# Kernel optimization log

Measured on AMD Instinct MI355X. Metric: run time of the kernel, lower is better.

Reference implementation:

```python
import jax, jax.numpy as jnp
import numpy as np

EPS = 1e-6  # torch GaussianNLLLoss default eps


def _linear_params(key, in_size, out_size):
    # torch nn.Linear default init: U(-1/sqrt(in), 1/sqrt(in)) for W and b
    kw, kb = jax.random.split(key)
    bound = 1.0 / np.sqrt(in_size)
    W = jax.random.uniform(kw, (out_size, in_size), minval=-bound, maxval=bound, dtype=jnp.float32)
    b = jax.random.uniform(kb, (out_size,), minval=-bound, maxval=bound, dtype=jnp.float32)
    return W, b


def setup_inputs() -> dict:
    key = jax.random.key(0)
    B, IN, H = 32768, 512, 512
    ks = jax.random.split(key, 6)
    x = jax.random.normal(ks[0], (B, IN), dtype=jnp.float32)
    y = jax.random.normal(ks[1], (B, IN), dtype=jnp.float32)
    W_mu_x, b_mu_x = _linear_params(ks[2], IN, H)
    W_sg_x, b_sg_x = _linear_params(ks[3], IN, H)
    W_mu_y, b_mu_y = _linear_params(ks[4], IN, H)
    W_sg_y, b_sg_y = _linear_params(ks[5], IN, H)
    return {"x": x, "y": y,
            "W_mu_x": W_mu_x, "b_mu_x": b_mu_x,
            "W_sg_x": W_sg_x, "b_sg_x": b_sg_x,
            "W_mu_y": W_mu_y, "b_mu_y": b_mu_y,
            "W_sg_y": W_sg_y, "b_sg_y": b_sg_y}


def _gaussian_nll(xi, mean, var):
    # torch GaussianNLLLoss (full=False, reduction='mean'):
    # mean over features of 0.5*(log(max(var,eps)) + (xi-mean)^2/max(var,eps))
    v = jnp.maximum(var, EPS)
    return 0.5 * jnp.mean(jnp.log(v) + (xi - mean) ** 2 / v)


def _sample_row(key, mx, my, vx, vy):
    # rejection sampling: draw u~U(0,1), xi~U(-1,1); accept when u >= q(xi)
    def cond(c):
        return jnp.logical_not(c[2])

    def body(c):
        k = c[0]
        k, k1, k2 = jax.random.split(k, 3)
        u = jax.random.uniform(k1, dtype=jnp.float32)
        xi = 2.0 * jax.random.uniform(k2, dtype=jnp.float32) - 1.0
        q = _gaussian_nll(xi, mx, vx) * _gaussian_nll(xi, my, vy)
        return (k, xi, u >= q)

    _, xi, _ = jax.lax.while_loop(cond, body, (key, jnp.float32(0.0), jnp.bool_(False)))
    return xi


def reference(x, y, W_mu_x, b_mu_x, W_sg_x, b_sg_x, W_mu_y, b_mu_y, W_sg_y, b_sg_y):
    mean_x = x @ W_mu_x.T + b_mu_x          # [B, H]
    mean_y = y @ W_mu_y.T + b_mu_y          # [B, H]
    std_x = jnp.exp(x @ W_sg_x.T + b_sg_x)  # [B, H] (used as 'var' in GaussianNLLLoss)
    std_y = jnp.exp(y @ W_sg_y.T + b_sg_y)  # [B, H]
    B = x.shape[0]
    keys = jax.random.split(jax.random.key(42), B)
    X = jax.vmap(_sample_row)(keys, mean_x, mean_y, std_x, std_y)  # [B]
    return jnp.clip(X, 1e-5, 10.0)
```

## Files before the change

kernel.cpp:

```cpp
#include <hip/hip_runtime.h>
#include <stdint.h>
#include <math.h>


typedef _Float16 f16;
typedef __attribute__((ext_vector_type(8))) _Float16 f16x8;
typedef __attribute__((ext_vector_type(4))) float f32x4;

#define SX 16.0f
#define SW 1024.0f
#define INV_S (1.0f / 16384.0f)
#define LOG_EPS (-13.815510557964274f)
#define WS_NEED (4u * 1024u * 1024u)

#define L_CJ    512
#define L_WV    1024
#define L_PL    4096
#define L_KS    16384
#define L_RID   32768

struct U2 { uint32_t a, b; };

__device__ __forceinline__ uint32_t rotl(uint32_t v, int d) {
  return (v << d) | (v >> (32 - d));
}

__device__ __forceinline__ U2 tf2x32(uint32_t k0, uint32_t k1, uint32_t x0, uint32_t x1) {
  const uint32_t k2 = k0 ^ k1 ^ 0x1BD11BDAu;
  x0 += k0; x1 += k1;
#define TFR(r) { x0 += x1; x1 = rotl(x1, r); x1 ^= x0; }
  TFR(13) TFR(15) TFR(26) TFR(6)
  x0 += k1; x1 += k2 + 1u;
  TFR(17) TFR(29) TFR(16) TFR(24)
  x0 += k2; x1 += k0 + 2u;
  TFR(13) TFR(15) TFR(26) TFR(6)
  x0 += k0; x1 += k1 + 3u;
  TFR(17) TFR(29) TFR(16) TFR(24)
  x0 += k1; x1 += k2 + 4u;
  TFR(13) TFR(15) TFR(26) TFR(6)
  x0 += k2; x1 += k0 + 5u;
#undef TFR
  U2 r; r.a = x0; r.b = x1; return r;
}

__device__ __forceinline__ float bits_to_u01(uint32_t b) {
  return __uint_as_float((b >> 9) | 0x3f800000u) - 1.0f;
}

__global__ __launch_bounds__(256) void convert_w_kernel(
    const float* __restrict__ w0, const float* __restrict__ w1,
    const float* __restrict__ w2, const float* __restrict__ w3,
    f16* __restrict__ ws)
{
  const int t = blockIdx.x * 256 + threadIdx.x;
  const int lane = t & 63;
  const int cj = (t >> 6) & 1;
  const int wv = (t >> 7) & 3;
  const int matsel = (t >> 9) & 1;
  const int ksub = (t >> 10) & 1;
  const int rid = t >> 11;
  const int dist = rid >> 5;
  const int cg = (rid >> 3) & 3;
  const int kc2 = rid & 7;

  const int mat = dist * 2 + matsel;
  const int row = cg * 128 + wv * 32 + cj * 16 + (lane & 15);
  const int k0 = kc2 * 64 + ksub * 32 + (lane >> 4) * 8;

  const float* W = (mat == 0) ? w0 : (mat == 1) ? w1 : (mat == 2) ? w2 : w3;
  const float* p = W + (size_t)row * 512 + k0;
  const float4 va = *(const float4*)p;
  const float4 vb = *(const float4*)(p + 4);
  const float a[8] = {va.x, va.y, va.z, va.w, vb.x, vb.y, vb.z, vb.w};
  f16x8 h, l;
#pragma unroll
  for (int i = 0; i < 8; ++i) {
    const float ai = a[i] * SW;
    const f16 hi = (f16)ai;
    h[i] = hi;
    l[i] = (f16)(ai - (float)hi);
  }
  f16* dst = ws + (size_t)rid * L_RID + (size_t)ksub * L_KS
                + (size_t)(matsel * 2) * L_PL + (size_t)wv * L_WV
                + (size_t)cj * L_CJ + (size_t)lane * 8;
  *(f16x8*)dst = h;
  *(f16x8*)(dst + L_PL) = l;
}

__device__ __forceinline__ int swz_off(int row, int quad) {
  return row * 32 + ((quad ^ ((row >> 1) & 3)) << 3);
}

__global__ __launch_bounds__(256, 2)
void mfma_proposal_kernel(const float* __restrict__ gx, const float* __restrict__ gy,
                          const float* __restrict__ bmux, const float* __restrict__ bsgx,
                          const float* __restrict__ bmuy, const float* __restrict__ bsgy,
                          const f16* __restrict__ ws, float* __restrict__ out)
{
  __shared__ f16 Xh[2][2][64 * 32];
  __shared__ f16 Xl[2][2][64 * 32];
  __shared__ double red[4][64][8];

  const int tid = threadIdx.x;
  const int lane = tid & 63;
  const int w = tid >> 6;
  const int ln = lane & 15;
  const int quad = lane >> 4;
  const int r0 = blockIdx.x * 64;

  const int xrow = tid >> 2;
  const int xs4 = tid & 3;
  const int xslot = (xs4 ^ ((xrow >> 1) & 3)) << 3;

  for (int i = tid; i < 4 * 64 * 8; i += 256) (&red[0][0][0])[i] = 0.0;

  float4 xr0a, xr0b, xr1a, xr1b;

  auto load_xr = [&](int n) {
    const float* Xg = (n >> 5) ? gy : gx;
    const float* xp = Xg + (size_t)(r0 + xrow) * 512 + (n & 7) * 64 + xs4 * 8;
    xr0a = *(const float4*)(xp);
    xr0b = *(const float4*)(xp + 4);
    xr1a = *(const float4*)(xp + 32);
    xr1b = *(const float4*)(xp + 36);
  };

  auto write_x = [&](int buf) {
#pragma unroll
    for (int s = 0; s < 2; ++s) {
      const float4 ra = s ? xr1a : xr0a;
      const float4 rb = s ? xr1b : xr0b;
      float a0 = ra.x * SX, a1 = ra.y * SX, a2 = ra.z * SX, a3 = ra.w * SX;
      float a4 = rb.x * SX, a5 = rb.y * SX, a6 = rb.z * SX, a7 = rb.w * SX;
      f16 h0 = (f16)a0, h1 = (f16)a1, h2 = (f16)a2, h3 = (f16)a3;
      f16 h4 = (f16)a4, h5 = (f16)a5, h6 = (f16)a6, h7 = (f16)a7;
      *(f16x8*)&Xh[buf][s][xrow * 32 + xslot] = (f16x8){h0, h1, h2, h3, h4, h5, h6, h7};
      *(f16x8*)&Xl[buf][s][xrow * 32 + xslot] =
          (f16x8){(f16)(a0 - (float)h0), (f16)(a1 - (float)h1),
                  (f16)(a2 - (float)h2), (f16)(a3 - (float)h3),
                  (f16)(a4 - (float)h4), (f16)(a5 - (float)h5),
                  (f16)(a6 - (float)h6), (f16)(a7 - (float)h7)};
    }
  };

  f32x4 accm[4][2], accv[4][2];

  load_xr(0);
  write_x(0);
  load_xr(1);

  for (int rid = 0; rid < 64; ++rid) {
    const int cb = rid & 1;
    const int kc2 = rid & 7;
    const int cg = (rid >> 3) & 3;
    const int dist = rid >> 5;

    if (kc2 == 0) {
#pragma unroll
      for (int ri = 0; ri < 4; ++ri)
#pragma unroll
        for (int cj = 0; cj < 2; ++cj) {
          accm[ri][cj] = (f32x4)0.0f;
          accv[ri][cj] = (f32x4)0.0f;
        }
    }

    __syncthreads();

    const f16* wr = ws + (size_t)rid * L_RID + (size_t)w * L_WV + (size_t)lane * 8;
    f16x8 B0[4][2], B1[4][2];
#pragma unroll
    for (int p = 0; p < 4; ++p)
#pragma unroll
      for (int cj = 0; cj < 2; ++cj) {
        B0[p][cj] = *(const f16x8*)(wr + (size_t)p * L_PL + (size_t)cj * L_CJ);
        B1[p][cj] = *(const f16x8*)(wr + L_KS + (size_t)p * L_PL + (size_t)cj * L_CJ);
      }

    if (rid + 1 < 64) write_x(cb ^ 1);
    if (rid + 2 < 64) load_xr(rid + 2);

#pragma unroll
    for (int s = 0; s < 2; ++s) {
      f16x8 ah[4], al[4];
#pragma unroll
      for (int ri = 0; ri < 4; ++ri) {
        const int off = swz_off(ri * 16 + ln, quad);
        ah[ri] = *(const f16x8*)&Xh[cb][s][off];
        al[ri] = *(const f16x8*)&Xl[cb][s][off];
      }
      __builtin_amdgcn_s_setprio(1);
#pragma unroll
      for (int cj = 0; cj < 2; ++cj) {
        const f16x8 bhm = s ? B1[0][cj] : B0[0][cj];
        const f16x8 blm = s ? B1[1][cj] : B0[1][cj];
        const f16x8 bhv = s ? B1[2][cj] : B0[2][cj];
        const f16x8 blv = s ? B1[3][cj] : B0[3][cj];
#pragma unroll
        for (int ri = 0; ri < 4; ++ri) {
          accm[ri][cj] = __builtin_amdgcn_mfma_f32_16x16x32_f16(al[ri], bhm, accm[ri][cj], 0, 0, 0);
          accm[ri][cj] = __builtin_amdgcn_mfma_f32_16x16x32_f16(ah[ri], blm, accm[ri][cj], 0, 0, 0);
          accm[ri][cj] = __builtin_amdgcn_mfma_f32_16x16x32_f16(ah[ri], bhm, accm[ri][cj], 0, 0, 0);
          accv[ri][cj] = __builtin_amdgcn_mfma_f32_16x16x32_f16(al[ri], bhv, accv[ri][cj], 0, 0, 0);
          accv[ri][cj] = __builtin_amdgcn_mfma_f32_16x16x32_f16(ah[ri], blv, accv[ri][cj], 0, 0, 0);
          accv[ri][cj] = __builtin_amdgcn_mfma_f32_16x16x32_f16(ah[ri], bhv, accv[ri][cj], 0, 0, 0);
        }
      }
      __builtin_amdgcn_s_setprio(0);
    }

    if (kc2 == 7) {
      const float* bmu = dist ? bmuy : bmux;
      const float* bsg = dist ? bsgy : bsgx;
      float bm0 = bmu[cg * 128 + w * 32 + ln];
      float bm1 = bmu[cg * 128 + w * 32 + 16 + ln];
      float bv0 = bsg[cg * 128 + w * 32 + ln];
      float bv1 = bsg[cg * 128 + w * 32 + 16 + ln];
#pragma unroll
      for (int ri = 0; ri < 4; ++ri) {
#pragma unroll
        for (int g = 0; g < 4; ++g) {
          float pA = 0.f, pI = 0.f, pM = 0.f, pQ = 0.f;
#pragma unroll
          for (int cj = 0; cj < 2; ++cj) {
            const float m = accm[ri][cj][g] * INV_S + (cj ? bm1 : bm0);
            const float s = accv[ri][cj][g] * INV_S + (cj ? bv1 : bv0);
            const float vv = fmaxf(expf(s), 1e-6f);
            const float lg = fmaxf(s, LOG_EPS);
            const float iv = __builtin_amdgcn_rcpf(vv);
            pA += lg;
            pI += iv;
            pM += m * iv;
            pQ += m * m * iv;
          }
#pragma unroll
          for (int msk = 1; msk < 16; msk <<= 1) {
            pA += __shfl_xor(pA, msk);
            pI += __shfl_xor(pI, msk);
            pM += __shfl_xor(pM, msk);
            pQ += __shfl_xor(pQ, msk);
          }
          if (ln == 0) {
            double* rr = &red[w][ri * 16 + quad * 4 + g][dist * 4];
            rr[0] += (double)pA; rr[1] += (double)pI;
            rr[2] += (double)pM; rr[3] += (double)pQ;
          }
        }
      }
    }
  }

  __syncthreads();

  if (tid < 64) {
    const int grow = r0 + tid;
    double Ax = 0, Ix = 0, Mx = 0, Qx = 0, Ay = 0, Iy = 0, My = 0, Qy = 0;
#pragma unroll
    for (int s = 0; s < 4; ++s) {
      Ax += red[s][tid][0]; Ix += red[s][tid][1];
      Mx += red[s][tid][2]; Qx += red[s][tid][3];
      Ay += red[s][tid][4]; Iy += red[s][tid][5];
      My += red[s][tid][6]; Qy += red[s][tid][7];
    }

    U2 key = tf2x32(0u, 42u, 0u, (uint32_t)grow);

    float xi = 0.0f;
    bool done = false;
    for (int it = 0; it < 100000 && !done; ++it) {
      const U2 kn = tf2x32(key.a, key.b, 0u, 0u);
      const U2 k1 = tf2x32(key.a, key.b, 0u, 1u);
      const U2 k2 = tf2x32(key.a, key.b, 0u, 2u);
      const U2 ru = tf2x32(k1.a, k1.b, 0u, 0u);
      const U2 rx = tf2x32(k2.a, k2.b, 0u, 0u);
      const float u  = bits_to_u01(ru.a ^ ru.b);
      const float u2 = bits_to_u01(rx.a ^ rx.b);
      xi = 2.0f * u2 - 1.0f;
      const double dxi = (double)xi;
      const double nx = (0.5 / 512.0) * (Ax + Qx + dxi * (dxi * Ix - 2.0 * Mx));
      const double ny = (0.5 / 512.0) * (Ay + Qy + dxi * (dxi * Iy - 2.0 * My));
      done = ((double)u >= nx * ny);
      key = kn;
    }
    out[grow] = fminf(fmaxf(xi, 1e-5f), 10.0f);
  }
}

__global__ __launch_bounds__(256, 1)
void fused_proposal_vec(const float* __restrict__ gx, const float* __restrict__ gy,
                        const float* __restrict__ Wmux, const float* __restrict__ bmux,
                        const float* __restrict__ Wsgx, const float* __restrict__ bsgx,
                        const float* __restrict__ Wmuy, const float* __restrict__ bmuy,
                        const float* __restrict__ Wsgy, const float* __restrict__ bsgy,
                        float* __restrict__ out)
{
  __shared__ float Xs[16][68];
  __shared__ float Wms[16][132];
  __shared__ float Wss[16][132];
  __shared__ double red[64][8];

  const int tid = threadIdx.x;
  const int tx = tid & 15;
  const int ty = tid >> 4;
  const int r0 = blockIdx.x * 64;
  const int lr = tid >> 2;
  const int q4 = (tid & 3) << 2;

  for (int i = tid; i < 64 * 8; i += 256) ((double*)red)[i] = 0.0;

  for (int ph = 0; ph < 8; ++ph) {
    const int dist = ph >> 2;
    const int c0 = (ph & 3) * 128;
    const float* __restrict__ Xg = dist ? gy : gx;
    const float* __restrict__ Wm = dist ? Wmuy : Wmux;
    const float* __restrict__ Wv = dist ? Wsgy : Wsgx;
    const float* __restrict__ bm = dist ? bmuy : bmux;
    const float* __restrict__ bv = dist ? bsgy : bsgx;

    float am[4][8], av[4][8];
#pragma unroll
    for (int r = 0; r < 4; ++r)
#pragma unroll
      for (int c = 0; c < 8; ++c) { am[r][c] = 0.0f; av[r][c] = 0.0f; }

    const float* xp  = Xg + (size_t)(r0 + lr) * 512 + q4;
    const float* mp0 = Wm + (size_t)(c0 + lr) * 512 + q4;
    const float* mp1 = Wm + (size_t)(c0 + lr + 64) * 512 + q4;
    const float* vp0 = Wv + (size_t)(c0 + lr) * 512 + q4;
    const float* vp1 = Wv + (size_t)(c0 + lr + 64) * 512 + q4;

    float4 xa = *(const float4*)(xp);
    float4 ma = *(const float4*)(mp0);
    float4 mb = *(const float4*)(mp1);
    float4 va = *(const float4*)(vp0);
    float4 vb = *(const float4*)(vp1);

    for (int t = 0; t < 32; ++t) {
      __syncthreads();
#define ST4(arr, col, v) { arr[q4+0][col]=v.x; arr[q4+1][col]=v.y; arr[q4+2][col]=v.z; arr[q4+3][col]=v.w; }
      ST4(Xs,  lr, xa)
      ST4(Wms, lr, ma)  ST4(Wms, lr + 64, mb)
      ST4(Wss, lr, va)  ST4(Wss, lr + 64, vb)
#undef ST4
      __syncthreads();
      if (t + 1 < 32) {
        const int ko = (t + 1) * 16;
        xa = *(const float4*)(xp + ko);
        ma = *(const float4*)(mp0 + ko);
        mb = *(const float4*)(mp1 + ko);
        va = *(const float4*)(vp0 + ko);
        vb = *(const float4*)(vp1 + ko);
      }
#pragma unroll
      for (int kk = 0; kk < 16; ++kk) {
        const float4 x0 = *(const float4*)&Xs[kk][ty * 4];
        const float4 m0 = *(const float4*)&Wms[kk][tx * 4];
        const float4 m1 = *(const float4*)&Wms[kk][tx * 4 + 64];
        const float4 v0 = *(const float4*)&Wss[kk][tx * 4];
        const float4 v1 = *(const float4*)&Wss[kk][tx * 4 + 64];
        const float xr[4] = {x0.x, x0.y, x0.z, x0.w};
        const float wm[8] = {m0.x, m0.y, m0.z, m0.w, m1.x, m1.y, m1.z, m1.w};
        const float wv[8] = {v0.x, v0.y, v0.z, v0.w, v1.x, v1.y, v1.z, v1.w};
#pragma unroll
        for (int r = 0; r < 4; ++r)
#pragma unroll
          for (int c = 0; c < 8; ++c) {
            am[r][c] = fmaf(xr[r], wm[c], am[r][c]);
            av[r][c] = fmaf(xr[r], wv[c], av[r][c]);
          }
      }
    }

    float bmr[8], bvr[8];
#pragma unroll
    for (int c = 0; c < 4; ++c) {
      bmr[c]     = bm[c0 + tx * 4 + c];
      bmr[4 + c] = bm[c0 + 64 + tx * 4 + c];
      bvr[c]     = bv[c0 + tx * 4 + c];
      bvr[4 + c] = bv[c0 + 64 + tx * 4 + c];
    }
#pragma unroll
    for (int r = 0; r < 4; ++r) {
      float pA = 0.f, pI = 0.f, pM = 0.f, pQ = 0.f;
#pragma unroll
      for (int c = 0; c < 8; ++c) {
        const float m = am[r][c] + bmr[c];
        const float s = av[r][c] + bvr[c];
        const float v = fmaxf(expf(s), 1e-6f);
        const float lg = fmaxf(s, LOG_EPS);
        const float inv = __builtin_amdgcn_rcpf(v);
        pA += lg; pI += inv; pM += m * inv; pQ += m * m * inv;
      }
#pragma unroll
      for (int msk = 1; msk < 16; msk <<= 1) {
        pA += __shfl_xor(pA, msk);
        pI += __shfl_xor(pI, msk);
        pM += __shfl_xor(pM, msk);
        pQ += __shfl_xor(pQ, msk);
      }
      if (tx == 0) {
        double* rr = &red[ty * 4 + r][dist * 4];
        rr[0] += (double)pA; rr[1] += (double)pI;
        rr[2] += (double)pM; rr[3] += (double)pQ;
      }
    }
  }

  __syncthreads();

  if (tid < 64) {
    const int grow = r0 + tid;
    const double Ax = red[tid][0], Ix = red[tid][1], Mx = red[tid][2], Qx = red[tid][3];
    const double Ay = red[tid][4], Iy = red[tid][5], My = red[tid][6], Qy = red[tid][7];
    U2 key = tf2x32(0u, 42u, 0u, (uint32_t)grow);
    float xi = 0.0f;
    bool done = false;
    for (int it = 0; it < 100000 && !done; ++it) {
      const U2 kn = tf2x32(key.a, key.b, 0u, 0u);
      const U2 k1 = tf2x32(key.a, key.b, 0u, 1u);
      const U2 k2 = tf2x32(key.a, key.b, 0u, 2u);
      const U2 ru = tf2x32(k1.a, k1.b, 0u, 0u);
      const U2 rx = tf2x32(k2.a, k2.b, 0u, 0u);
      const float u  = bits_to_u01(ru.a ^ ru.b);
      const float u2 = bits_to_u01(rx.a ^ rx.b);
      xi = 2.0f * u2 - 1.0f;
      const double dxi = (double)xi;
      const double nx = (0.5 / 512.0) * (Ax + Qx + dxi * (dxi * Ix - 2.0 * Mx));
      const double ny = (0.5 / 512.0) * (Ay + Qy + dxi * (dxi * Iy - 2.0 * My));
      done = ((double)u >= nx * ny);
      key = kn;
    }
    out[grow] = fminf(fmaxf(xi, 1e-5f), 10.0f);
  }
}

extern "C" void kernel_launch(void* const* d_in, const int* in_sizes, int n_in,
                              void* d_out, int out_size, void* d_ws, size_t ws_size,
                              hipStream_t stream) {
  const float* x    = (const float*)d_in[0];
  const float* y    = (const float*)d_in[1];
  const float* Wmux = (const float*)d_in[2];
  const float* bmux = (const float*)d_in[3];
  const float* Wsgx = (const float*)d_in[4];
  const float* bsgx = (const float*)d_in[5];
  const float* Wmuy = (const float*)d_in[6];
  const float* bmuy = (const float*)d_in[7];
  const float* Wsgy = (const float*)d_in[8];
  const float* bsgy = (const float*)d_in[9];
  (void)in_sizes; (void)n_in; (void)out_size;

  if (ws_size >= (size_t)WS_NEED) {
    convert_w_kernel<<<512, 256, 0, stream>>>(Wmux, Wsgx, Wmuy, Wsgy, (f16*)d_ws);
    mfma_proposal_kernel<<<512, 256, 0, stream>>>(
        x, y, bmux, bsgx, bmuy, bsgy, (const f16*)d_ws, (float*)d_out);
  } else {
    fused_proposal_vec<<<512, 256, 0, stream>>>(
        x, y, Wmux, bmux, Wsgx, bsgx, Wmuy, bmuy, Wsgy, bsgy, (float*)d_out);
  }
}
```

Measured before the change: 355.6 us.

## Stage half-K X slabs in LDS and double-buffer weight fragments in registers

Replaces the per-step double-buffered 64-wide X staging with phases that convert a 64x256 half-row slab of X into LDS once, separated by two barriers per phase. Weight fragments are reordered into 32-K blocks and prefetched one step ahead into a register double buffer, so each K step needs only one B load set. The aim is fewer barriers and better hiding of weight-load latency. The cost is larger LDS use, which may lower occupancy, an exposed X-load stall at each phase start, and removal of the setprio hints.

```diff
diff --git a/kernel.cpp b/kernel.cpp
--- a/kernel.cpp
+++ b/kernel.cpp
@@ -13,11 +13,10 @@
 #define LOG_EPS (-13.815510557964274f)
 #define WS_NEED (4u * 1024u * 1024u)
 
-#define L_CJ    512
-#define L_WV    1024
-#define L_PL    4096
-#define L_KS    16384
-#define L_RID   32768
+#define B_CJ   512
+#define B_PL   1024
+#define B_WV   4096
+#define B_RID  16384
 
 struct U2 { uint32_t a, b; };
 
@@ -55,17 +54,16 @@
   const int t = blockIdx.x * 256 + threadIdx.x;
   const int lane = t & 63;
   const int cj = (t >> 6) & 1;
-  const int wv = (t >> 7) & 3;
-  const int matsel = (t >> 9) & 1;
-  const int ksub = (t >> 10) & 1;
-  const int rid = t >> 11;
-  const int dist = rid >> 5;
-  const int cg = (rid >> 3) & 3;
-  const int kc2 = rid & 7;
+  const int matsel = (t >> 7) & 1;
+  const int wv = (t >> 8) & 3;
+  const int rid = t >> 10;
+  const int dist = rid >> 6;
+  const int cg = (rid >> 4) & 3;
+  const int kc = rid & 15;
 
   const int mat = dist * 2 + matsel;
   const int row = cg * 128 + wv * 32 + cj * 16 + (lane & 15);
-  const int k0 = kc2 * 64 + ksub * 32 + (lane >> 4) * 8;
+  const int k0 = kc * 32 + (lane >> 4) * 8;
 
   const float* W = (mat == 0) ? w0 : (mat == 1) ? w1 : (mat == 2) ? w2 : w3;
   const float* p = W + (size_t)row * 512 + k0;
@@ -80,15 +78,11 @@
     h[i] = hi;
     l[i] = (f16)(ai - (float)hi);
   }
-  f16* dst = ws + (size_t)rid * L_RID + (size_t)ksub * L_KS
-                + (size_t)(matsel * 2) * L_PL + (size_t)wv * L_WV
-                + (size_t)cj * L_CJ + (size_t)lane * 8;
+  f16* dst = ws + (size_t)rid * B_RID + (size_t)wv * B_WV
+                + (size_t)(matsel * 2) * B_PL + (size_t)cj * B_CJ
+                + (size_t)lane * 8;
   *(f16x8*)dst = h;
-  *(f16x8*)(dst + L_PL) = l;
-}
-
-__device__ __forceinline__ int swz_off(int row, int quad) {
-  return row * 32 + ((quad ^ ((row >> 1) & 3)) << 3);
+  *(f16x8*)(dst + B_PL) = l;
 }
 
 __global__ __launch_bounds__(256, 2)
@@ -97,8 +91,8 @@
                           const float* __restrict__ bmuy, const float* __restrict__ bsgy,
                           const f16* __restrict__ ws, float* __restrict__ out)
 {
-  __shared__ f16 Xh[2][2][64 * 32];
-  __shared__ f16 Xl[2][2][64 * 32];
+  __shared__ f16 Xh[64 * 256];
+  __shared__ f16 Xl[64 * 256];
   __shared__ double red[4][64][8];
 
   const int tid = threadIdx.x;
@@ -108,94 +102,90 @@
   const int quad = lane >> 4;
   const int r0 = blockIdx.x * 64;
 
-  const int xrow = tid >> 2;
-  const int xs4 = tid & 3;
-  const int xslot = (xs4 ^ ((xrow >> 1) & 3)) << 3;
-
   for (int i = tid; i < 4 * 64 * 8; i += 256) (&red[0][0][0])[i] = 0.0;
 
-  float4 xr0a, xr0b, xr1a, xr1b;
-
-  auto load_xr = [&](int n) {
-    const float* Xg = (n >> 5) ? gy : gx;
-    const float* xp = Xg + (size_t)(r0 + xrow) * 512 + (n & 7) * 64 + xs4 * 8;
-    xr0a = *(const float4*)(xp);
-    xr0b = *(const float4*)(xp + 4);
-    xr1a = *(const float4*)(xp + 32);
-    xr1b = *(const float4*)(xp + 36);
-  };
-
-  auto write_x = [&](int buf) {
-#pragma unroll
-    for (int s = 0; s < 2; ++s) {
-      const float4 ra = s ? xr1a : xr0a;
-      const float4 rb = s ? xr1b : xr0b;
-      float a0 = ra.x * SX, a1 = ra.y * SX, a2 = ra.z * SX, a3 = ra.w * SX;
-      float a4 = rb.x * SX, a5 = rb.y * SX, a6 = rb.z * SX, a7 = rb.w * SX;
-      f16 h0 = (f16)a0, h1 = (f16)a1, h2 = (f16)a2, h3 = (f16)a3;
-      f16 h4 = (f16)a4, h5 = (f16)a5, h6 = (f16)a6, h7 = (f16)a7;
-      *(f16x8*)&Xh[buf][s][xrow * 32 + xslot] = (f16x8){h0, h1, h2, h3, h4, h5, h6, h7};
-      *(f16x8*)&Xl[buf][s][xrow * 32 + xslot] =
-          (f16x8){(f16)(a0 - (float)h0), (f16)(a1 - (float)h1),
-                  (f16)(a2 - (float)h2), (f16)(a3 - (float)h3),
-                  (f16)(a4 - (float)h4), (f16)(a5 - (float)h5),
-                  (f16)(a6 - (float)h6), (f16)(a7 - (float)h7)};
-    }
-  };
+  const f16* wb = ws + (size_t)w * B_WV + (size_t)lane * 8;
+
+  f16x8 B[2][4][2];
+#pragma unroll
+  for (int p = 0; p < 4; ++p)
+#pragma unroll
+    for (int cj = 0; cj < 2; ++cj)
+      B[0][p][cj] = *(const f16x8*)(wb + p * B_PL + cj * B_CJ);
 
   f32x4 accm[4][2], accv[4][2];
 
-  load_xr(0);
-  write_x(0);
-  load_xr(1);
-
-  for (int rid = 0; rid < 64; ++rid) {
-    const int cb = rid & 1;
-    const int kc2 = rid & 7;
-    const int cg = (rid >> 3) & 3;
-    const int dist = rid >> 5;
-
-    if (kc2 == 0) {
-#pragma unroll
-      for (int ri = 0; ri < 4; ++ri)
-#pragma unroll
-        for (int cj = 0; cj < 2; ++cj) {
-          accm[ri][cj] = (f32x4)0.0f;
-          accv[ri][cj] = (f32x4)0.0f;
-        }
-    }
+  for (int ph = 0; ph < 16; ++ph) {
+    const int dist = ph >> 3;
+    const int cg = (ph >> 1) & 3;
+    const int kh = ph & 1;
 
     __syncthreads();
-
-    const f16* wr = ws + (size_t)rid * L_RID + (size_t)w * L_WV + (size_t)lane * 8;
-    f16x8 B0[4][2], B1[4][2];
-#pragma unroll
-    for (int p = 0; p < 4; ++p)
+    {
+      const float* __restrict__ Xg = dist ? gy : gx;
+#pragma unroll
+      for (int it = 0; it < 8; ++it) {
+        const int v = it * 256 + tid;
+        const int row = v >> 5;
+        const int sl = v & 31;
+        const float* p = Xg + (size_t)(r0 + row) * 512 + kh * 256 + sl * 8;
+        const float4 va = *(const float4*)p;
+        const float4 vb = *(const float4*)(p + 4);
+        float a0 = va.x * SX, a1 = va.y * SX, a2 = va.z * SX, a3 = va.w * SX;
+        float a4 = vb.x * SX, a5 = vb.y * SX, a6 = vb.z * SX, a7 = vb.w * SX;
+        f16 h0 = (f16)a0, h1 = (f16)a1, h2 = (f16)a2, h3 = (f16)a3;
+        f16 h4 = (f16)a4, h5 = (f16)a5, h6 = (f16)a6, h7 = (f16)a7;
+        const int so = row * 256 + ((sl ^ (row & 7)) << 3);
+        *(f16x8*)&Xh[so] = (f16x8){h0, h1, h2, h3, h4, h5, h6, h7};
+        *(f16x8*)&Xl[so] =
+            (f16x8){(f16)(a0 - (float)h0), (f16)(a1 - (float)h1),
+                    (f16)(a2 - (float)h2), (f16)(a3 - (float)h3),
+                    (f16)(a4 - (float)h4), (f16)(a5 - (float)h5),
+                    (f16)(a6 - (float)h6), (f16)(a7 - (float)h7)};
+      }
+    }
+    __syncthreads();
+
+#pragma unroll
+    for (int kcw = 0; kcw < 8; ++kcw) {
+      const int rid = ph * 8 + kcw;
+      const int cur = kcw & 1;
+
+      if (kh == 0 && kcw == 0) {
+#pragma unroll
+        for (int ri = 0; ri < 4; ++ri)
+#pragma unroll
+          for (int cj = 0; cj < 2; ++cj) {
+            accm[ri][cj] = (f32x4)0.0f;
+            accv[ri][cj] = (f32x4)0.0f;
+          }
+      }
+
+      if (kcw < 7 || ph < 15) {
+        const f16* nb = ws + (size_t)(rid + 1) * B_RID + (size_t)w * B_WV
+                           + (size_t)lane * 8;
+#pragma unroll
+        for (int p = 0; p < 4; ++p)
+#pragma unroll
+          for (int cj = 0; cj < 2; ++cj)
+            B[cur ^ 1][p][cj] = *(const f16x8*)(nb + p * B_PL + cj * B_CJ);
+      }
+
+      f16x8 ah[4], al[4];
+#pragma unroll
+      for (int ri = 0; ri < 4; ++ri) {
+        const int row = ri * 16 + ln;
+        const int so = row * 256 + (((kcw * 4 + quad) ^ (row & 7)) << 3);
+        ah[ri] = *(const f16x8*)&Xh[so];
+        al[ri] = *(const f16x8*)&Xl[so];
+      }
+
 #pragma unroll
       for (int cj = 0; cj < 2; ++cj) {
-        B0[p][cj] = *(const f16x8*)(wr + (size_t)p * L_PL + (size_t)cj * L_CJ);
-        B1[p][cj] = *(const f16x8*)(wr + L_KS + (size_t)p * L_PL + (size_t)cj * L_CJ);
-      }
-
-    if (rid + 1 < 64) write_x(cb ^ 1);
-    if (rid + 2 < 64) load_xr(rid + 2);
-
-#pragma unroll
-    for (int s = 0; s < 2; ++s) {
-      f16x8 ah[4], al[4];
-#pragma unroll
-      for (int ri = 0; ri < 4; ++ri) {
-        const int off = swz_off(ri * 16 + ln, quad);
-        ah[ri] = *(const f16x8*)&Xh[cb][s][off];
-        al[ri] = *(const f16x8*)&Xl[cb][s][off];
-      }
-      __builtin_amdgcn_s_setprio(1);
-#pragma unroll
-      for (int cj = 0; cj < 2; ++cj) {
-        const f16x8 bhm = s ? B1[0][cj] : B0[0][cj];
-        const f16x8 blm = s ? B1[1][cj] : B0[1][cj];
-        const f16x8 bhv = s ? B1[2][cj] : B0[2][cj];
-        const f16x8 blv = s ? B1[3][cj] : B0[3][cj];
+        const f16x8 bhm = B[cur][0][cj];
+        const f16x8 blm = B[cur][1][cj];
+        const f16x8 bhv = B[cur][2][cj];
+        const f16x8 blv = B[cur][3][cj];
 #pragma unroll
         for (int ri = 0; ri < 4; ++ri) {
           accm[ri][cj] = __builtin_amdgcn_mfma_f32_16x16x32_f16(al[ri], bhm, accm[ri][cj], 0, 0, 0);
@@ -206,44 +196,43 @@
           accv[ri][cj] = __builtin_amdgcn_mfma_f32_16x16x32_f16(ah[ri], bhv, accv[ri][cj], 0, 0, 0);
         }
       }
-      __builtin_amdgcn_s_setprio(0);
-    }
-
-    if (kc2 == 7) {
-      const float* bmu = dist ? bmuy : bmux;
-      const float* bsg = dist ? bsgy : bsgx;
-      float bm0 = bmu[cg * 128 + w * 32 + ln];
-      float bm1 = bmu[cg * 128 + w * 32 + 16 + ln];
-      float bv0 = bsg[cg * 128 + w * 32 + ln];
-      float bv1 = bsg[cg * 128 + w * 32 + 16 + ln];
-#pragma unroll
-      for (int ri = 0; ri < 4; ++ri) {
-#pragma unroll
-        for (int g = 0; g < 4; ++g) {
-          float pA = 0.f, pI = 0.f, pM = 0.f, pQ = 0.f;
-#pragma unroll
-          for (int cj = 0; cj < 2; ++cj) {
-            const float m = accm[ri][cj][g] * INV_S + (cj ? bm1 : bm0);
-            const float s = accv[ri][cj][g] * INV_S + (cj ? bv1 : bv0);
-            const float vv = fmaxf(expf(s), 1e-6f);
-            const float lg = fmaxf(s, LOG_EPS);
-            const float iv = __builtin_amdgcn_rcpf(vv);
-            pA += lg;
-            pI += iv;
-            pM += m * iv;
-            pQ += m * m * iv;
-          }
-#pragma unroll
-          for (int msk = 1; msk < 16; msk <<= 1) {
-            pA += __shfl_xor(pA, msk);
-            pI += __shfl_xor(pI, msk);
-            pM += __shfl_xor(pM, msk);
-            pQ += __shfl_xor(pQ, msk);
-          }
-          if (ln == 0) {
-            double* rr = &red[w][ri * 16 + quad * 4 + g][dist * 4];
-            rr[0] += (double)pA; rr[1] += (double)pI;
-            rr[2] += (double)pM; rr[3] += (double)pQ;
+
+      if (kh == 1 && kcw == 7) {
+        const float* bmu = dist ? bmuy : bmux;
+        const float* bsg = dist ? bsgy : bsgx;
+        float bm0 = bmu[cg * 128 + w * 32 + ln];
+        float bm1 = bmu[cg * 128 + w * 32 + 16 + ln];
+        float bv0 = bsg[cg * 128 + w * 32 + ln];
+        float bv1 = bsg[cg * 128 + w * 32 + 16 + ln];
+#pragma unroll
+        for (int ri = 0; ri < 4; ++ri) {
+#pragma unroll
+          for (int g = 0; g < 4; ++g) {
+            float pA = 0.f, pI = 0.f, pM = 0.f, pQ = 0.f;
+#pragma unroll
+            for (int cj = 0; cj < 2; ++cj) {
+              const float m = accm[ri][cj][g] * INV_S + (cj ? bm1 : bm0);
+              const float s = accv[ri][cj][g] * INV_S + (cj ? bv1 : bv0);
+              const float vv = fmaxf(expf(s), 1e-6f);
+              const float lg = fmaxf(s, LOG_EPS);
+              const float iv = __builtin_amdgcn_rcpf(vv);
+              pA += lg;
+              pI += iv;
+              pM += m * iv;
+              pQ += m * m * iv;
+            }
+#pragma unroll
+            for (int msk = 1; msk < 16; msk <<= 1) {
+              pA += __shfl_xor(pA, msk);
+              pI += __shfl_xor(pI, msk);
+              pM += __shfl_xor(pM, msk);
+              pQ += __shfl_xor(pQ, msk);
+            }
+            if (ln == 0) {
+              double* rr = &red[w][ri * 16 + quad * 4 + g][dist * 4];
+              rr[0] += (double)pA; rr[1] += (double)pI;
+              rr[2] += (double)pM; rr[3] += (double)pQ;
+            }
           }
         }
       }
```

Result: slower. 371.3 us (+4.4%).

## Switch split-fp16 GEMM from 16x16x32 to 32x32x16 MFMA tiles

Applied to the files above, without the earlier changes.

Replaces the 16x16x32 MFMA tiling with 32x32x16 MFMA instructions, so each wave computes two 32x32 output tiles per matrix instead of eight 16x16 tiles. The pre-converted weight layout and the LDS fragment addressing change to match the new operand shapes. This cuts the number of MFMA issues and A-fragment LDS reads per k-step. In exchange the epilogue reduction now needs a 5-step cross-lane shuffle per accumulator register instead of 4 steps, and there are more registers to reduce.

```diff
diff --git a/kernel.cpp b/kernel.cpp
--- a/kernel.cpp
+++ b/kernel.cpp
@@ -5,7 +5,7 @@
 
 typedef _Float16 f16;
 typedef __attribute__((ext_vector_type(8))) _Float16 f16x8;
-typedef __attribute__((ext_vector_type(4))) float f32x4;
+typedef __attribute__((ext_vector_type(16))) float f32x16;
 
 #define SX 16.0f
 #define SW 1024.0f
@@ -13,11 +13,11 @@
 #define LOG_EPS (-13.815510557964274f)
 #define WS_NEED (4u * 1024u * 1024u)
 
-#define L_CJ    512
-#define L_WV    1024
-#define L_PL    4096
-#define L_KS    16384
-#define L_RID   32768
+#define B_PL   512
+#define B_WV   2048
+#define B_KS   8192
+#define B_KSUB 16384
+#define B_RID  32768
 
 struct U2 { uint32_t a, b; };
 
@@ -53,22 +53,12 @@
     f16* __restrict__ ws)
 {
   const int t = blockIdx.x * 256 + threadIdx.x;
-  const int lane = t & 63;
-  const int cj = (t >> 6) & 1;
-  const int wv = (t >> 7) & 3;
-  const int matsel = (t >> 9) & 1;
-  const int ksub = (t >> 10) & 1;
-  const int rid = t >> 11;
-  const int dist = rid >> 5;
-  const int cg = (rid >> 3) & 3;
-  const int kc2 = rid & 7;
-
-  const int mat = dist * 2 + matsel;
-  const int row = cg * 128 + wv * 32 + cj * 16 + (lane & 15);
-  const int k0 = kc2 * 64 + ksub * 32 + (lane >> 4) * 8;
+  const int k8 = t & 63;
+  const int row = (t >> 6) & 511;
+  const int mat = t >> 15;
 
   const float* W = (mat == 0) ? w0 : (mat == 1) ? w1 : (mat == 2) ? w2 : w3;
-  const float* p = W + (size_t)row * 512 + k0;
+  const float* p = W + (size_t)row * 512 + k8 * 8;
   const float4 va = *(const float4*)p;
   const float4 vb = *(const float4*)(p + 4);
   const float a[8] = {va.x, va.y, va.z, va.w, vb.x, vb.y, vb.z, vb.w};
@@ -80,15 +70,18 @@
     h[i] = hi;
     l[i] = (f16)(ai - (float)hi);
   }
-  f16* dst = ws + (size_t)rid * L_RID + (size_t)ksub * L_KS
-                + (size_t)(matsel * 2) * L_PL + (size_t)wv * L_WV
-                + (size_t)cj * L_CJ + (size_t)lane * 8;
+
+  const int dist = mat >> 1, matsel = mat & 1;
+  const int cg = row >> 7, wv = (row >> 5) & 3;
+  const int kc2 = k8 >> 3, ksub = (k8 >> 2) & 1, ks = (k8 >> 1) & 1;
+  const int lane = (row & 31) + 32 * (k8 & 1);
+  const int rid = dist * 32 + cg * 8 + kc2;
+
+  f16* dst = ws + (size_t)rid * B_RID + (size_t)ksub * B_KSUB
+                + (size_t)ks * B_KS + (size_t)wv * B_WV
+                + (size_t)(matsel * 2) * B_PL + (size_t)lane * 8;
   *(f16x8*)dst = h;
-  *(f16x8*)(dst + L_PL) = l;
-}
-
-__device__ __forceinline__ int swz_off(int row, int quad) {
-  return row * 32 + ((quad ^ ((row >> 1) & 3)) << 3);
+  *(f16x8*)(dst + B_PL) = l;
 }
 
 __global__ __launch_bounds__(256, 2)
@@ -104,8 +97,8 @@
   const int tid = threadIdx.x;
   const int lane = tid & 63;
   const int w = tid >> 6;
-  const int ln = lane & 15;
-  const int quad = lane >> 4;
+  const int l31 = lane & 31;
+  const int lh = lane >> 5;
   const int r0 = blockIdx.x * 64;
 
   const int xrow = tid >> 2;
@@ -143,7 +136,7 @@
     }
   };
 
-  f32x4 accm[4][2], accv[4][2];
+  f32x16 accm[2], accv[2];
 
   load_xr(0);
   write_x(0);
@@ -157,91 +150,86 @@
 
     if (kc2 == 0) {
 #pragma unroll
-      for (int ri = 0; ri < 4; ++ri)
-#pragma unroll
-        for (int cj = 0; cj < 2; ++cj) {
-          accm[ri][cj] = (f32x4)0.0f;
-          accv[ri][cj] = (f32x4)0.0f;
-        }
+      for (int t = 0; t < 2; ++t) {
+        accm[t] = (f32x16)0.0f;
+        accv[t] = (f32x16)0.0f;
+      }
     }
 
     __syncthreads();
 
-    const f16* wr = ws + (size_t)rid * L_RID + (size_t)w * L_WV + (size_t)lane * 8;
-    f16x8 B0[4][2], B1[4][2];
-#pragma unroll
-    for (int p = 0; p < 4; ++p)
-#pragma unroll
-      for (int cj = 0; cj < 2; ++cj) {
-        B0[p][cj] = *(const f16x8*)(wr + (size_t)p * L_PL + (size_t)cj * L_CJ);
-        B1[p][cj] = *(const f16x8*)(wr + L_KS + (size_t)p * L_PL + (size_t)cj * L_CJ);
-      }
+    const f16* wr = ws + (size_t)rid * B_RID + (size_t)w * B_WV + (size_t)lane * 8;
+    f16x8 Bf[2][2][4];
+#pragma unroll
+    for (int su = 0; su < 2; ++su)
+#pragma unroll
+      for (int ks = 0; ks < 2; ++ks)
+#pragma unroll
+        for (int p = 0; p < 4; ++p)
+          Bf[su][ks][p] = *(const f16x8*)(wr + (size_t)su * B_KSUB
+                                             + (size_t)ks * B_KS
+                                             + (size_t)p * B_PL);
 
     if (rid + 1 < 64) write_x(cb ^ 1);
     if (rid + 2 < 64) load_xr(rid + 2);
 
 #pragma unroll
-    for (int s = 0; s < 2; ++s) {
-      f16x8 ah[4], al[4];
-#pragma unroll
-      for (int ri = 0; ri < 4; ++ri) {
-        const int off = swz_off(ri * 16 + ln, quad);
-        ah[ri] = *(const f16x8*)&Xh[cb][s][off];
-        al[ri] = *(const f16x8*)&Xl[cb][s][off];
-      }
-      __builtin_amdgcn_s_setprio(1);
-#pragma unroll
-      for (int cj = 0; cj < 2; ++cj) {
-        const f16x8 bhm = s ? B1[0][cj] : B0[0][cj];
-        const f16x8 blm = s ? B1[1][cj] : B0[1][cj];
-        const f16x8 bhv = s ? B1[2][cj] : B0[2][cj];
-        const f16x8 blv = s ? B1[3][cj] : B0[3][cj];
-#pragma unroll
-        for (int ri = 0; ri < 4; ++ri) {
-          accm[ri][cj] = __builtin_amdgcn_mfma_f32_16x16x32_f16(al[ri], bhm, accm[ri][cj], 0, 0, 0);
-          accm[ri][cj] = __builtin_amdgcn_mfma_f32_16x16x32_f16(ah[ri], blm, accm[ri][cj], 0, 0, 0);
-          accm[ri][cj] = __builtin_amdgcn_mfma_f32_16x16x32_f16(ah[ri], bhm, accm[ri][cj], 0, 0, 0);
-          accv[ri][cj] = __builtin_amdgcn_mfma_f32_16x16x32_f16(al[ri], bhv, accv[ri][cj], 0, 0, 0);
-          accv[ri][cj] = __builtin_amdgcn_mfma_f32_16x16x32_f16(ah[ri], blv, accv[ri][cj], 0, 0, 0);
-          accv[ri][cj] = __builtin_amdgcn_mfma_f32_16x16x32_f16(ah[ri], bhv, accv[ri][cj], 0, 0, 0);
+    for (int su = 0; su < 2; ++su) {
+#pragma unroll
+      for (int ks = 0; ks < 2; ++ks) {
+        f16x8 ah[2], al[2];
+#pragma unroll
+        for (int t = 0; t < 2; ++t) {
+          const int row = t * 32 + l31;
+          const int slot = (2 * ks + lh) ^ ((row >> 1) & 3);
+          const int off = row * 32 + slot * 8;
+          ah[t] = *(const f16x8*)&Xh[cb][su][off];
+          al[t] = *(const f16x8*)&Xl[cb][su][off];
         }
-      }
-      __builtin_amdgcn_s_setprio(0);
+        const f16x8 bhm = Bf[su][ks][0];
+        const f16x8 blm = Bf[su][ks][1];
+        const f16x8 bhv = Bf[su][ks][2];
+        const f16x8 blv = Bf[su][ks][3];
+        __builtin_amdgcn_s_setprio(1);
+#pragma unroll
+        for (int t = 0; t < 2; ++t) {
+          accm[t] = __builtin_amdgcn_mfma_f32_32x32x16_f16(al[t], bhm, accm[t], 0, 0, 0);
+          accm[t] = __builtin_amdgcn_mfma_f32_32x32x16_f16(ah[t], blm, accm[t], 0, 0, 0);
+          accm[t] = __builtin_amdgcn_mfma_f32_32x32x16_f16(ah[t], bhm, accm[t], 0, 0, 0);
+          accv[t] = __builtin_amdgcn_mfma_f32_32x32x16_f16(al[t], bhv, accv[t], 0, 0, 0);
+          accv[t] = __builtin_amdgcn_mfma_f32_32x32x16_f16(ah[t], blv, accv[t], 0, 0, 0);
+          accv[t] = __builtin_amdgcn_mfma_f32_32x32x16_f16(ah[t], bhv, accv[t], 0, 0, 0);
+        }
+        __builtin_amdgcn_s_setprio(0);
+      }
     }
 
     if (kc2 == 7) {
       const float* bmu = dist ? bmuy : bmux;
       const float* bsg = dist ? bsgy : bsgx;
-      float bm0 = bmu[cg * 128 + w * 32 + ln];
-      float bm1 = bmu[cg * 128 + w * 32 + 16 + ln];
-      float bv0 = bsg[cg * 128 + w * 32 + ln];
-      float bv1 = bsg[cg * 128 + w * 32 + 16 + ln];
-#pragma unroll
-      for (int ri = 0; ri < 4; ++ri) {
-#pragma unroll
-        for (int g = 0; g < 4; ++g) {
-          float pA = 0.f, pI = 0.f, pM = 0.f, pQ = 0.f;
-#pragma unroll
-          for (int cj = 0; cj < 2; ++cj) {
-            const float m = accm[ri][cj][g] * INV_S + (cj ? bm1 : bm0);
-            const float s = accv[ri][cj][g] * INV_S + (cj ? bv1 : bv0);
-            const float vv = fmaxf(expf(s), 1e-6f);
-            const float lg = fmaxf(s, LOG_EPS);
-            const float iv = __builtin_amdgcn_rcpf(vv);
-            pA += lg;
-            pI += iv;
-            pM += m * iv;
-            pQ += m * m * iv;
-          }
-#pragma unroll
-          for (int msk = 1; msk < 16; msk <<= 1) {
+      const int col = cg * 128 + w * 32 + l31;
+      const float bm = bmu[col];
+      const float bv = bsg[col];
+#pragma unroll
+      for (int t = 0; t < 2; ++t) {
+#pragma unroll
+        for (int reg = 0; reg < 16; ++reg) {
+          const float m = accm[t][reg] * INV_S + bm;
+          const float s_ = accv[t][reg] * INV_S + bv;
+          const float vv = fmaxf(expf(s_), 1e-6f);
+          const float lg = fmaxf(s_, LOG_EPS);
+          const float iv = __builtin_amdgcn_rcpf(vv);
+          float pA = lg, pI = iv, pM = m * iv, pQ = m * m * iv;
+#pragma unroll
+          for (int msk = 1; msk < 32; msk <<= 1) {
             pA += __shfl_xor(pA, msk);
             pI += __shfl_xor(pI, msk);
             pM += __shfl_xor(pM, msk);
             pQ += __shfl_xor(pQ, msk);
           }
-          if (ln == 0) {
-            double* rr = &red[w][ri * 16 + quad * 4 + g][dist * 4];
+          if (l31 == 0) {
+            const int row = t * 32 + (reg & 3) + 8 * (reg >> 2) + 4 * lh;
+            double* rr = &red[w][row][dist * 4];
             rr[0] += (double)pA; rr[1] += (double)pI;
             rr[2] += (double)pM; rr[3] += (double)pQ;
           }
```

After: 428.1 us. +20.4%, slower.
